# Optimization experiments

Measured on AMD Instinct MI355X. Metric: run time of the kernel, lower is better.

The kernel has to match this reference:

```python
import jax, jax.numpy as jnp
import numpy as np

DIM = 128
HEADS = 4
DIM_HEAD = 32
HIDDEN = HEADS * DIM_HEAD
SCALE = DIM_HEAD ** -0.5
EPS = 1e-5


def setup_inputs() -> dict:
    key = jax.random.key(0)
    ks = jax.random.split(key, 8)
    s = 1.0 / np.sqrt(DIM)
    x = jax.random.normal(ks[0], (32, DIM, 64, 64), dtype=jnp.float32)
    Wq = jax.random.uniform(ks[1], (HIDDEN, DIM), jnp.float32, -s, s)
    Wk = jax.random.uniform(ks[2], (HIDDEN, DIM), jnp.float32, -s, s)
    Wv = jax.random.uniform(ks[3], (HIDDEN, DIM), jnp.float32, -s, s)
    so = 1.0 / np.sqrt(HIDDEN)
    Wo = jax.random.uniform(ks[4], (DIM, HIDDEN), jnp.float32, -so, so)
    bo = jax.random.uniform(ks[5], (DIM,), jnp.float32, -so, so)
    gn_w = jnp.ones((DIM,), jnp.float32)
    gn_b = jnp.zeros((DIM,), jnp.float32)
    return {"x": x, "Wq": Wq, "Wk": Wk, "Wv": Wv, "Wo": Wo, "bo": bo,
            "gn_w": gn_w, "gn_b": gn_b}


def reference(x, Wq, Wk, Wv, Wo, bo, gn_w, gn_b):
    b, c, h, w = x.shape
    n = h * w
    xf = x.reshape(b, c, n)  # [b, c, n]
    # 1x1 convs (no bias) == channel matmuls; split heads: [b, H, d, n]
    def proj(W):
        return jnp.einsum('oc,bcn->bon', W, xf).reshape(b, HEADS, DIM_HEAD, n)
    q = proj(Wq)
    k = proj(Wk)
    v = proj(Wv)
    q = jax.nn.softmax(q, axis=-2) * SCALE  # softmax over head-dim d
    k = jax.nn.softmax(k, axis=-1)          # softmax over spatial n
    ctx = jnp.einsum('bhdn,bhen->bhde', k, v)   # [b,H,d,e], tiny d=e=32
    out = jnp.einsum('bhde,bhdn->bhen', ctx, q) # [b,H,e,n]
    out = out.reshape(b, HIDDEN, n)
    # output 1x1 conv with bias
    out = jnp.einsum('oc,bcn->bon', Wo, out) + bo[None, :, None]  # [b,dim,n]
    # GroupNorm(num_groups=1): normalize over (C, n) per sample
    mu = jnp.mean(out, axis=(1, 2), keepdims=True)
    var = jnp.var(out, axis=(1, 2), keepdims=True)
    out = (out - mu) * jax.lax.rsqrt(var + EPS)
    out = out * gn_w[None, :, None] + gn_b[None, :, None]
    return out.reshape(b, c, h, w)
```

## Files before the change

kernel.cpp:

```cpp
#include <hip/hip_runtime.h>


#define B_   32
#define C_   128
#define N_   4096
#define H_   4
#define D_   32
#define HID  128
#define NB   64
#define TPB  4
#define NSTRIP 16
#define STV  72
#define STA  136
#define SCT  40
#define SCALE 0.1767766952966369f
#define EPS  1e-5f

typedef __attribute__((ext_vector_type(8))) short short8;
typedef __attribute__((ext_vector_type(4))) short short4v;
typedef __attribute__((ext_vector_type(4))) float floatx4;

__device__ __forceinline__ short f2bf(float f) {
  unsigned u = __float_as_uint(f);
  u += 0x7FFFu + ((u >> 16) & 1u);
  return (short)(u >> 16);
}
__device__ __forceinline__ float bf2f(short h) {
  return __uint_as_float(((unsigned)(unsigned short)h) << 16);
}
__device__ __forceinline__ void gload_lds16(const float* g, void* l) {
  __builtin_amdgcn_global_load_lds(
      (const __attribute__((address_space(1))) unsigned int*)g,
      (__attribute__((address_space(3))) unsigned int*)l, 16, 0, 0);
}

__global__ __launch_bounds__(256) void k_wcast(
    const float* __restrict__ Wq, const float* __restrict__ Wk,
    const float* __restrict__ Wv, const float* __restrict__ Wo,
    short* __restrict__ wb) {
  const int i = blockIdx.x * 256 + threadIdx.x;
  const float* srcs[4] = {Wq, Wk, Wv, Wo};
#pragma unroll
  for (int m = 0; m < 4; ++m) {
    floatx4 a = ((const floatx4*)srcs[m])[i];
    short4v s = { f2bf(a[0]), f2bf(a[1]), f2bf(a[2]), f2bf(a[3]) };
    ((short4v*)(wb + m * 16384))[i] = s;
  }
}

__global__ __launch_bounds__(256, 2) void k_kv_ctx(
    const float* __restrict__ x, const short* __restrict__ Wkb,
    const short* __restrict__ Wvb, float* __restrict__ ctx_u,
    float* __restrict__ Zsum) {
  __shared__ float natx[C_ * NB];
  __shared__ short ekbuf[C_ * STV];
  __shared__ short vbuf [C_ * STV];
  const int tid = threadIdx.x;
  const int w = tid >> 6, L = tid & 63, l15 = tid & 15, q4 = (tid & 63) >> 4;
  const int b = blockIdx.x / NSTRIP;
  const int strip = blockIdx.x % NSTRIP;
  const float* xb = x + (size_t)b * C_ * N_;

  short8 ak[2][4], av[2][4];
#pragma unroll
  for (int mt = 0; mt < 2; ++mt)
#pragma unroll
    for (int ks = 0; ks < 4; ++ks) {
      ak[mt][ks] = *(const short8*)&Wkb[(w * 32 + mt * 16 + l15) * C_ + ks * 32 + q4 * 8];
      av[mt][ks] = *(const short8*)&Wvb[(w * 32 + mt * 16 + l15) * C_ + ks * 32 + q4 * 8];
    }

  const floatx4 z4 = {0.f, 0.f, 0.f, 0.f};
  floatx4 ca[2][2] = {{z4, z4}, {z4, z4}};
  float zreg[2][4] = {{0.f,0.f,0.f,0.f},{0.f,0.f,0.f,0.f}};

#pragma unroll
  for (int i = 0; i < 8; ++i) {
    const int c = w * 32 + i * 4 + (L >> 4);
    gload_lds16(xb + (size_t)c * N_ + (size_t)(strip * TPB) * NB + (L & 15) * 4,
                (char*)natx + ((w * 32 + i * 4) * NB + L * 4) * 4);
  }

  for (int t = 0; t < TPB; ++t) {
    __syncthreads();

    floatx4 acck[2][4], accv[2][4];
#pragma unroll
    for (int mt = 0; mt < 2; ++mt)
#pragma unroll
      for (int nt = 0; nt < 4; ++nt) { acck[mt][nt] = z4; accv[mt][nt] = z4; }

#pragma unroll
    for (int ks = 0; ks < 4; ++ks) {
      short8 Bf[4];
#pragma unroll
      for (int nt = 0; nt < 4; ++nt) {
        short8 s;
#pragma unroll
        for (int j = 0; j < 8; ++j)
          s[j] = f2bf(natx[(ks * 32 + q4 * 8 + j) * NB + nt * 16 + l15]);
        Bf[nt] = s;
      }
#pragma unroll
      for (int mt = 0; mt < 2; ++mt)
#pragma unroll
        for (int nt = 0; nt < 4; ++nt) {
          acck[mt][nt] = __builtin_amdgcn_mfma_f32_16x16x32_bf16(ak[mt][ks], Bf[nt], acck[mt][nt], 0, 0, 0);
          accv[mt][nt] = __builtin_amdgcn_mfma_f32_16x16x32_bf16(av[mt][ks], Bf[nt], accv[mt][nt], 0, 0, 0);
        }
    }
    __syncthreads();

    if (t + 1 < TPB) {
#pragma unroll
      for (int i = 0; i < 8; ++i) {
        const int c = w * 32 + i * 4 + (L >> 4);
        gload_lds16(xb + (size_t)c * N_ + (size_t)(strip * TPB + t + 1) * NB + (L & 15) * 4,
                    (char*)natx + ((w * 32 + i * 4) * NB + L * 4) * 4);
      }
    }

#pragma unroll
    for (int mt = 0; mt < 2; ++mt)
#pragma unroll
      for (int nt = 0; nt < 4; ++nt)
#pragma unroll
        for (int r = 0; r < 4; ++r)
          acck[mt][nt][r] = __expf(acck[mt][nt][r]);
#pragma unroll
    for (int mt = 0; mt < 2; ++mt)
#pragma unroll
      for (int r = 0; r < 4; ++r)
        zreg[mt][r] += acck[mt][0][r] + acck[mt][1][r] + acck[mt][2][r] + acck[mt][3][r];

#pragma unroll
    for (int mt = 0; mt < 2; ++mt)
#pragma unroll
      for (int nt = 0; nt < 4; ++nt)
#pragma unroll
        for (int r = 0; r < 4; ++r) {
          ekbuf[(w * 32 + mt * 16 + q4 * 4 + r) * STV + nt * 16 + l15] = f2bf(acck[mt][nt][r]);
          vbuf [(w * 32 + mt * 16 + q4 * 4 + r) * STV + nt * 16 + l15] = f2bf(accv[mt][nt][r]);
        }

#pragma unroll
    for (int ks = 0; ks < 2; ++ks) {
      short8 ae[2], be[2];
#pragma unroll
      for (int mt = 0; mt < 2; ++mt)
        ae[mt] = *(const short8*)&ekbuf[(w * 32 + mt * 16 + l15) * STV + ks * 32 + q4 * 8];
#pragma unroll
      for (int nt = 0; nt < 2; ++nt)
        be[nt] = *(const short8*)&vbuf[(w * 32 + nt * 16 + l15) * STV + ks * 32 + q4 * 8];
#pragma unroll
      for (int mt = 0; mt < 2; ++mt)
#pragma unroll
        for (int nt = 0; nt < 2; ++nt)
          ca[mt][nt] = __builtin_amdgcn_mfma_f32_16x16x32_bf16(ae[mt], be[nt], ca[mt][nt], 0, 0, 0);
    }
  }

#pragma unroll
  for (int mt = 0; mt < 2; ++mt)
#pragma unroll
    for (int r = 0; r < 4; ++r) {
      float s = zreg[mt][r];
      s += __shfl_xor(s, 1); s += __shfl_xor(s, 2);
      s += __shfl_xor(s, 4); s += __shfl_xor(s, 8);
      if (l15 == 0) atomicAdd(&Zsum[b * HID + w * 32 + mt * 16 + q4 * 4 + r], s);
    }

  float* cb = &ctx_u[((size_t)b * H_ + w) * (D_ * D_)];
#pragma unroll
  for (int mt = 0; mt < 2; ++mt)
#pragma unroll
    for (int nt = 0; nt < 2; ++nt)
#pragma unroll
      for (int r = 0; r < 4; ++r)
        atomicAdd(&cb[(mt * 16 + q4 * 4 + r) * D_ + nt * 16 + l15], ca[mt][nt][r]);
}

__global__ __launch_bounds__(256, 2) void k_q_attn_o(
    const float* __restrict__ x, const short* __restrict__ Wqb,
    const short* __restrict__ Wob, const float* __restrict__ bo,
    const float* __restrict__ ctx_u, const float* __restrict__ Zsum,
    float* __restrict__ outp, float* __restrict__ stats) {
  __shared__ float natx[C_ * NB];
  __shared__ short qat[NB * STA];
  __shared__ short ctxT[HID * SCT];
  const int tid = threadIdx.x;
  const int w = tid >> 6, L = tid & 63, l15 = tid & 15, q4 = (tid & 63) >> 4;
  const int b = blockIdx.x / NSTRIP;
  const int strip = blockIdx.x % NSTRIP;
  const float* xb = x + (size_t)b * C_ * N_;

#pragma unroll
  for (int i = 0; i < 8; ++i) {
    const int c = w * 32 + i * 4 + (L >> 4);
    gload_lds16(xb + (size_t)c * N_ + (size_t)(strip * TPB) * NB + (L & 15) * 4,
                (char*)natx + ((w * 32 + i * 4) * NB + L * 4) * 4);
  }
#pragma unroll
  for (int i = 0; i < 16; ++i) {
    const int idx = tid + i * 256;
    float v = ctx_u[(size_t)b * (H_ * D_ * D_) + idx] *
              __builtin_amdgcn_rcpf(Zsum[b * HID + (idx >> 5)]);
    ctxT[((idx >> 10) * 32 + (idx & 31)) * SCT + ((idx >> 5) & 31)] = f2bf(v);
  }

  short8 aq[2][4], ao[2][4];
#pragma unroll
  for (int mt = 0; mt < 2; ++mt)
#pragma unroll
    for (int ks = 0; ks < 4; ++ks) {
      aq[mt][ks] = *(const short8*)&Wqb[(w * 32 + mt * 16 + l15) * C_ + ks * 32 + q4 * 8];
      ao[mt][ks] = *(const short8*)&Wob[(w * 32 + mt * 16 + l15) * HID + ks * 32 + q4 * 8];
    }

  const floatx4 z4 = {0.f, 0.f, 0.f, 0.f};
  float s1 = 0.f, s2 = 0.f;

  for (int t = 0; t < TPB; ++t) {
    const int n0 = (strip * TPB + t) * NB;
    __syncthreads();

    floatx4 acc[2][4];
#pragma unroll
    for (int mt = 0; mt < 2; ++mt)
#pragma unroll
      for (int nt = 0; nt < 4; ++nt) acc[mt][nt] = z4;
#pragma unroll
    for (int ks = 0; ks < 4; ++ks) {
      short8 Bf[4];
#pragma unroll
      for (int nt = 0; nt < 4; ++nt) {
        short8 s;
#pragma unroll
        for (int j = 0; j < 8; ++j)
          s[j] = f2bf(natx[(ks * 32 + q4 * 8 + j) * NB + nt * 16 + l15]);
        Bf[nt] = s;
      }
#pragma unroll
      for (int mt = 0; mt < 2; ++mt)
#pragma unroll
        for (int nt = 0; nt < 4; ++nt)
          acc[mt][nt] = __builtin_amdgcn_mfma_f32_16x16x32_bf16(aq[mt][ks], Bf[nt], acc[mt][nt], 0, 0, 0);
    }
    __syncthreads();

    if (t + 1 < TPB) {
#pragma unroll
      for (int i = 0; i < 8; ++i) {
        const int c = w * 32 + i * 4 + (L >> 4);
        gload_lds16(xb + (size_t)c * N_ + (size_t)(n0 + NB) + (L & 15) * 4,
                    (char*)natx + ((w * 32 + i * 4) * NB + L * 4) * 4);
      }
    }

#pragma unroll
    for (int mt = 0; mt < 2; ++mt)
#pragma unroll
      for (int nt = 0; nt < 4; ++nt)
#pragma unroll
        for (int r = 0; r < 4; ++r)
          acc[mt][nt][r] = __expf(acc[mt][nt][r]);
    float inv[4];
#pragma unroll
    for (int nt = 0; nt < 4; ++nt) {
      float s = 0.f;
#pragma unroll
      for (int mt = 0; mt < 2; ++mt)
#pragma unroll
        for (int r = 0; r < 4; ++r) s += acc[mt][nt][r];
      s += __shfl_xor(s, 16); s += __shfl_xor(s, 32);
      inv[nt] = SCALE * __builtin_amdgcn_rcpf(s);
    }

#pragma unroll
    for (int mt = 0; mt < 2; ++mt)
#pragma unroll
      for (int nt = 0; nt < 4; ++nt) {
        short4v pk = { f2bf(acc[mt][nt][0] * inv[nt]), f2bf(acc[mt][nt][1] * inv[nt]),
                       f2bf(acc[mt][nt][2] * inv[nt]), f2bf(acc[mt][nt][3] * inv[nt]) };
        *(short4v*)&qat[(nt * 16 + l15) * STA + w * 32 + mt * 16 + q4 * 4] = pk;
      }

    {
      floatx4 aacc[2][4];
#pragma unroll
      for (int mt = 0; mt < 2; ++mt)
#pragma unroll
        for (int nt = 0; nt < 4; ++nt) aacc[mt][nt] = z4;
      short8 ae[2];
#pragma unroll
      for (int mt = 0; mt < 2; ++mt)
        ae[mt] = *(const short8*)&ctxT[(w * 32 + mt * 16 + l15) * SCT + q4 * 8];
#pragma unroll
      for (int nt = 0; nt < 4; ++nt) {
        short8 bq = *(const short8*)&qat[(nt * 16 + l15) * STA + w * 32 + q4 * 8];
#pragma unroll
        for (int mt = 0; mt < 2; ++mt)
          aacc[mt][nt] = __builtin_amdgcn_mfma_f32_16x16x32_bf16(ae[mt], bq, aacc[mt][nt], 0, 0, 0);
      }
#pragma unroll
      for (int nt = 0; nt < 4; ++nt)
#pragma unroll
        for (int mt = 0; mt < 2; ++mt) {
          short4v pk = { f2bf(aacc[mt][nt][0]), f2bf(aacc[mt][nt][1]),
                         f2bf(aacc[mt][nt][2]), f2bf(aacc[mt][nt][3]) };
          *(short4v*)&qat[(nt * 16 + l15) * STA + w * 32 + mt * 16 + q4 * 4] = pk;
        }
    }
    __syncthreads();

    floatx4 oacc[2][4];
#pragma unroll
    for (int mt = 0; mt < 2; ++mt)
#pragma unroll
      for (int nt = 0; nt < 4; ++nt) oacc[mt][nt] = z4;
#pragma unroll
    for (int ks = 0; ks < 4; ++ks) {
      short8 bf8[4];
#pragma unroll
      for (int nt = 0; nt < 4; ++nt)
        bf8[nt] = *(const short8*)&qat[(nt * 16 + l15) * STA + ks * 32 + q4 * 8];
#pragma unroll
      for (int mt = 0; mt < 2; ++mt)
#pragma unroll
        for (int nt = 0; nt < 4; ++nt)
          oacc[mt][nt] = __builtin_amdgcn_mfma_f32_16x16x32_bf16(ao[mt][ks], bf8[nt], oacc[mt][nt], 0, 0, 0);
    }

#pragma unroll
    for (int mt = 0; mt < 2; ++mt) {
      const int rowbase = w * 32 + mt * 16 + q4 * 4;
      const floatx4 bo4 = *(const floatx4*)&bo[rowbase];
#pragma unroll
      for (int nt = 0; nt < 4; ++nt) {
        const int n = n0 + nt * 16 + l15;
#pragma unroll
        for (int r = 0; r < 4; ++r) {
          float vv = oacc[mt][nt][r] + bo4[r];
          outp[(size_t)b * (C_ * N_) + (size_t)(rowbase + r) * N_ + n] = vv;
          s1 += vv; s2 += vv * vv;
        }
      }
    }
  }

#pragma unroll
  for (int m = 1; m < 64; m <<= 1) {
    s1 += __shfl_xor(s1, m);
    s2 += __shfl_xor(s2, m);
  }
  if ((tid & 63) == 0) {
    atomicAdd(&stats[b * 2 + 0], s1);
    atomicAdd(&stats[b * 2 + 1], s2);
  }
}

__global__ __launch_bounds__(256) void k_gnorm(
    float* __restrict__ outp, const float* __restrict__ stats,
    const float* __restrict__ gnw, const float* __restrict__ gnb) {
  const int b = blockIdx.x >> 6;
  const int blk = blockIdx.x & 63;
  const float M = (float)(C_ * N_);
  const float mu = stats[b * 2 + 0] / M;
  const float var = stats[b * 2 + 1] / M - mu * mu;
  const float rs = rsqrtf(var + EPS);
  floatx4* p = (floatx4*)(outp + (size_t)b * (C_ * N_) + (size_t)blk * 8192);
  const int tid = threadIdx.x;
#pragma unroll
  for (int i = 0; i < 8; ++i) {
    const int idx = tid + i * 256;
    const int fl = blk * 8192 + idx * 4;
    const int c = fl >> 12;
    const float wgt = gnw[c] * rs;
    const float bia = gnb[c] - mu * wgt;
    floatx4 v = p[idx];
    v[0] = v[0] * wgt + bia;
    v[1] = v[1] * wgt + bia;
    v[2] = v[2] * wgt + bia;
    v[3] = v[3] * wgt + bia;
    p[idx] = v;
  }
}

extern "C" void kernel_launch(void* const* d_in, const int* in_sizes, int n_in,
                              void* d_out, int out_size, void* d_ws, size_t ws_size,
                              hipStream_t stream) {
  (void)in_sizes; (void)n_in; (void)out_size; (void)ws_size;
  const float* x   = (const float*)d_in[0];
  const float* Wq  = (const float*)d_in[1];
  const float* Wk  = (const float*)d_in[2];
  const float* Wv  = (const float*)d_in[3];
  const float* Wo  = (const float*)d_in[4];
  const float* bo  = (const float*)d_in[5];
  const float* gnw = (const float*)d_in[6];
  const float* gnb = (const float*)d_in[7];
  float* outp  = (float*)d_out;
  float* ctx_u = (float*)d_ws;
  float* Zsum  = ctx_u + B_ * H_ * D_ * D_;
  float* stats = Zsum + B_ * HID;
  short* wb    = (short*)(stats + B_ * 2);
  const size_t zbytes = (size_t)(B_ * H_ * D_ * D_ + B_ * HID + B_ * 2) * sizeof(float);
  hipMemsetAsync(d_ws, 0, zbytes, stream);
  hipLaunchKernelGGL(k_wcast,    dim3(64),           dim3(256), 0, stream, Wq, Wk, Wv, Wo, wb);
  hipLaunchKernelGGL(k_kv_ctx,   dim3(B_ * NSTRIP),  dim3(256), 0, stream, x, wb + 16384, wb + 32768, ctx_u, Zsum);
  hipLaunchKernelGGL(k_q_attn_o, dim3(B_ * NSTRIP),  dim3(256), 0, stream, x, wb, wb + 49152, bo, ctx_u, Zsum, outp, stats);
  hipLaunchKernelGGL(k_gnorm,    dim3(B_ * 64),      dim3(256), 0, stream, outp, stats, gnw, gnb);
}
```

Baseline: 205.0 us.

## Stash swizzled bf16 transposed x in first pass for reuse by Q kernel

The KV/context kernel now writes its bf16-converted, transposed x tiles to a workspace buffer, and the Q/attention/output kernel reads that half-size buffer instead of re-reading and re-converting fp32 x. Both LDS layouts get an XOR swizzle to reduce bank conflicts. The second kernel uses smaller strips (more blocks) and a higher occupancy bound. This adds extra global writes in the first kernel and depends on the workspace being large enough, falling back to the legacy path otherwise.

```diff
diff --git a/kernel.cpp b/kernel.cpp
--- a/kernel.cpp
+++ b/kernel.cpp
@@ -10,6 +10,8 @@
 #define NB   64
 #define TPB  4
 #define NSTRIP 16
+#define TPB2   2
+#define NSTRIP2 32
 #define STV  72
 #define STA  136
 #define SCT  40
@@ -32,6 +34,9 @@
   __builtin_amdgcn_global_load_lds(
       (const __attribute__((address_space(1))) unsigned int*)g,
       (__attribute__((address_space(3))) unsigned int*)l, 16, 0, 0);
+}
+__device__ __forceinline__ int swzn(int c) {
+  return (((c >> 3) & 1) << 4) | (((c >> 4) & 1) << 3);
 }
 
 __global__ __launch_bounds__(256) void k_wcast(
@@ -51,7 +56,7 @@
 __global__ __launch_bounds__(256, 2) void k_kv_ctx(
     const float* __restrict__ x, const short* __restrict__ Wkb,
     const short* __restrict__ Wvb, float* __restrict__ ctx_u,
-    float* __restrict__ Zsum) {
+    float* __restrict__ Zsum, short* __restrict__ xt) {
   __shared__ float natx[C_ * NB];
   __shared__ short ekbuf[C_ * STV];
   __shared__ short vbuf [C_ * STV];
@@ -60,6 +65,8 @@
   const int b = blockIdx.x / NSTRIP;
   const int strip = blockIdx.x % NSTRIP;
   const float* xb = x + (size_t)b * C_ * N_;
+  const int szr = ((q4 & 1) << 4) | ((q4 & 2) << 2);
+  const int szw = (l15 & 7) << 3;
 
   short8 ak[2][4], av[2][4];
 #pragma unroll
@@ -77,7 +84,7 @@
 #pragma unroll
   for (int i = 0; i < 8; ++i) {
     const int c = w * 32 + i * 4 + (L >> 4);
-    gload_lds16(xb + (size_t)c * N_ + (size_t)(strip * TPB) * NB + (L & 15) * 4,
+    gload_lds16(xb + (size_t)c * N_ + (size_t)(strip * TPB) * NB + (((L & 15) * 4) ^ swzn(c)),
                 (char*)natx + ((w * 32 + i * 4) * NB + L * 4) * 4);
   }
 
@@ -90,6 +97,7 @@
 #pragma unroll
       for (int nt = 0; nt < 4; ++nt) { acck[mt][nt] = z4; accv[mt][nt] = z4; }
 
+    short8 myB[4];
 #pragma unroll
     for (int ks = 0; ks < 4; ++ks) {
       short8 Bf[4];
@@ -98,8 +106,11 @@
         short8 s;
 #pragma unroll
         for (int j = 0; j < 8; ++j)
-          s[j] = f2bf(natx[(ks * 32 + q4 * 8 + j) * NB + nt * 16 + l15]);
+          s[j] = f2bf(natx[(ks * 32 + q4 * 8 + j) * NB + ((nt * 16 + l15) ^ szr)]);
         Bf[nt] = s;
+      }
+      if (ks == w) {
+        myB[0] = Bf[0]; myB[1] = Bf[1]; myB[2] = Bf[2]; myB[3] = Bf[3];
       }
 #pragma unroll
       for (int mt = 0; mt < 2; ++mt)
@@ -115,9 +126,16 @@
 #pragma unroll
       for (int i = 0; i < 8; ++i) {
         const int c = w * 32 + i * 4 + (L >> 4);
-        gload_lds16(xb + (size_t)c * N_ + (size_t)(strip * TPB + t + 1) * NB + (L & 15) * 4,
+        gload_lds16(xb + (size_t)c * N_ + (size_t)(strip * TPB + t + 1) * NB + (((L & 15) * 4) ^ swzn(c)),
                     (char*)natx + ((w * 32 + i * 4) * NB + L * 4) * 4);
       }
+    }
+
+    if (xt) {
+      short* xtb = xt + ((size_t)(b * 64 + strip * TPB + t)) * 8192;
+#pragma unroll
+      for (int nt = 0; nt < 4; ++nt)
+        *(short8*)&xtb[(nt * 16 + l15) * C_ + ((w * 32 + q4 * 8) ^ szw)] = myB[nt];
     }
 
 #pragma unroll
@@ -180,7 +198,180 @@
         atomicAdd(&cb[(mt * 16 + q4 * 4 + r) * D_ + nt * 16 + l15], ca[mt][nt][r]);
 }
 
-__global__ __launch_bounds__(256, 2) void k_q_attn_o(
+__global__ __launch_bounds__(256, 3) void k_q_attn_o(
+    const short* __restrict__ xt, const short* __restrict__ Wqb,
+    const short* __restrict__ Wob, const float* __restrict__ bo,
+    const float* __restrict__ ctx_u, const float* __restrict__ Zsum,
+    float* __restrict__ outp, float* __restrict__ stats) {
+  __shared__ short natx2[NB * C_];
+  __shared__ short qat[NB * STA];
+  __shared__ short ctxT[HID * SCT];
+  const int tid = threadIdx.x;
+  const int w = tid >> 6, L = tid & 63, l15 = tid & 15, q4 = (tid & 63) >> 4;
+  const int b = blockIdx.x / NSTRIP2;
+  const int strip = blockIdx.x % NSTRIP2;
+  const int szw = (l15 & 7) << 3;
+  (void)L;
+
+  {
+    const float* src = (const float*)(xt + (size_t)(b * 64 + strip * TPB2) * 8192);
+#pragma unroll
+    for (int i = 0; i < 4; ++i)
+      gload_lds16(src + tid * 4 + i * 1024, (char*)natx2 + tid * 16 + i * 4096);
+  }
+#pragma unroll
+  for (int i = 0; i < 16; ++i) {
+    const int idx = tid + i * 256;
+    float v = ctx_u[(size_t)b * (H_ * D_ * D_) + idx] *
+              __builtin_amdgcn_rcpf(Zsum[b * HID + (idx >> 5)]);
+    ctxT[((idx >> 10) * 32 + (idx & 31)) * SCT + ((idx >> 5) & 31)] = f2bf(v);
+  }
+
+  short8 aq[2][4], ao[2][4];
+#pragma unroll
+  for (int mt = 0; mt < 2; ++mt)
+#pragma unroll
+    for (int ks = 0; ks < 4; ++ks) {
+      aq[mt][ks] = *(const short8*)&Wqb[(w * 32 + mt * 16 + l15) * C_ + ks * 32 + q4 * 8];
+      ao[mt][ks] = *(const short8*)&Wob[(w * 32 + mt * 16 + l15) * HID + ks * 32 + q4 * 8];
+    }
+
+  const floatx4 z4 = {0.f, 0.f, 0.f, 0.f};
+  float s1 = 0.f, s2 = 0.f;
+
+  for (int t = 0; t < TPB2; ++t) {
+    const int n0 = (strip * TPB2 + t) * NB;
+    __syncthreads();
+
+    floatx4 acc[2][4];
+#pragma unroll
+    for (int mt = 0; mt < 2; ++mt)
+#pragma unroll
+      for (int nt = 0; nt < 4; ++nt) acc[mt][nt] = z4;
+#pragma unroll
+    for (int ks = 0; ks < 4; ++ks) {
+      short8 Bf[4];
+#pragma unroll
+      for (int nt = 0; nt < 4; ++nt)
+        Bf[nt] = *(const short8*)&natx2[(nt * 16 + l15) * C_ + ((ks * 32 + q4 * 8) ^ szw)];
+#pragma unroll
+      for (int mt = 0; mt < 2; ++mt)
+#pragma unroll
+        for (int nt = 0; nt < 4; ++nt)
+          acc[mt][nt] = __builtin_amdgcn_mfma_f32_16x16x32_bf16(aq[mt][ks], Bf[nt], acc[mt][nt], 0, 0, 0);
+    }
+    __syncthreads();
+
+    if (t + 1 < TPB2) {
+      const float* src = (const float*)(xt + (size_t)(b * 64 + strip * TPB2 + t + 1) * 8192);
+#pragma unroll
+      for (int i = 0; i < 4; ++i)
+        gload_lds16(src + tid * 4 + i * 1024, (char*)natx2 + tid * 16 + i * 4096);
+    }
+
+#pragma unroll
+    for (int mt = 0; mt < 2; ++mt)
+#pragma unroll
+      for (int nt = 0; nt < 4; ++nt)
+#pragma unroll
+        for (int r = 0; r < 4; ++r)
+          acc[mt][nt][r] = __expf(acc[mt][nt][r]);
+    float inv[4];
+#pragma unroll
+    for (int nt = 0; nt < 4; ++nt) {
+      float s = 0.f;
+#pragma unroll
+      for (int mt = 0; mt < 2; ++mt)
+#pragma unroll
+        for (int r = 0; r < 4; ++r) s += acc[mt][nt][r];
+      s += __shfl_xor(s, 16); s += __shfl_xor(s, 32);
+      inv[nt] = SCALE * __builtin_amdgcn_rcpf(s);
+    }
+
+#pragma unroll
+    for (int mt = 0; mt < 2; ++mt)
+#pragma unroll
+      for (int nt = 0; nt < 4; ++nt) {
+        short4v pk = { f2bf(acc[mt][nt][0] * inv[nt]), f2bf(acc[mt][nt][1] * inv[nt]),
+                       f2bf(acc[mt][nt][2] * inv[nt]), f2bf(acc[mt][nt][3] * inv[nt]) };
+        *(short4v*)&qat[(nt * 16 + l15) * STA + w * 32 + mt * 16 + q4 * 4] = pk;
+      }
+
+    {
+      floatx4 aacc[2][4];
+#pragma unroll
+      for (int mt = 0; mt < 2; ++mt)
+#pragma unroll
+        for (int nt = 0; nt < 4; ++nt) aacc[mt][nt] = z4;
+      short8 ae[2];
+#pragma unroll
+      for (int mt = 0; mt < 2; ++mt)
+        ae[mt] = *(const short8*)&ctxT[(w * 32 + mt * 16 + l15) * SCT + q4 * 8];
+#pragma unroll
+      for (int nt = 0; nt < 4; ++nt) {
+        short8 bq = *(const short8*)&qat[(nt * 16 + l15) * STA + w * 32 + q4 * 8];
+#pragma unroll
+        for (int mt = 0; mt < 2; ++mt)
+          aacc[mt][nt] = __builtin_amdgcn_mfma_f32_16x16x32_bf16(ae[mt], bq, aacc[mt][nt], 0, 0, 0);
+      }
+#pragma unroll
+      for (int nt = 0; nt < 4; ++nt)
+#pragma unroll
+        for (int mt = 0; mt < 2; ++mt) {
+          short4v pk = { f2bf(aacc[mt][nt][0]), f2bf(aacc[mt][nt][1]),
+                         f2bf(aacc[mt][nt][2]), f2bf(aacc[mt][nt][3]) };
+          *(short4v*)&qat[(nt * 16 + l15) * STA + w * 32 + mt * 16 + q4 * 4] = pk;
+        }
+    }
+    __syncthreads();
+
+    floatx4 oacc[2][4];
+#pragma unroll
+    for (int mt = 0; mt < 2; ++mt)
+#pragma unroll
+      for (int nt = 0; nt < 4; ++nt) oacc[mt][nt] = z4;
+#pragma unroll
+    for (int ks = 0; ks < 4; ++ks) {
+      short8 bf8[4];
+#pragma unroll
+      for (int nt = 0; nt < 4; ++nt)
+        bf8[nt] = *(const short8*)&qat[(nt * 16 + l15) * STA + ks * 32 + q4 * 8];
+#pragma unroll
+      for (int mt = 0; mt < 2; ++mt)
+#pragma unroll
+        for (int nt = 0; nt < 4; ++nt)
+          oacc[mt][nt] = __builtin_amdgcn_mfma_f32_16x16x32_bf16(ao[mt][ks], bf8[nt], oacc[mt][nt], 0, 0, 0);
+    }
+
+#pragma unroll
+    for (int mt = 0; mt < 2; ++mt) {
+      const int rowbase = w * 32 + mt * 16 + q4 * 4;
+      const floatx4 bo4 = *(const floatx4*)&bo[rowbase];
+#pragma unroll
+      for (int nt = 0; nt < 4; ++nt) {
+        const int n = n0 + nt * 16 + l15;
+#pragma unroll
+        for (int r = 0; r < 4; ++r) {
+          float vv = oacc[mt][nt][r] + bo4[r];
+          outp[(size_t)b * (C_ * N_) + (size_t)(rowbase + r) * N_ + n] = vv;
+          s1 += vv; s2 += vv * vv;
+        }
+      }
+    }
+  }
+
+#pragma unroll
+  for (int m = 1; m < 64; m <<= 1) {
+    s1 += __shfl_xor(s1, m);
+    s2 += __shfl_xor(s2, m);
+  }
+  if ((tid & 63) == 0) {
+    atomicAdd(&stats[b * 2 + 0], s1);
+    atomicAdd(&stats[b * 2 + 1], s2);
+  }
+}
+
+__global__ __launch_bounds__(256, 2) void k_q_attn_o_legacy(
     const float* __restrict__ x, const short* __restrict__ Wqb,
     const short* __restrict__ Wob, const float* __restrict__ bo,
     const float* __restrict__ ctx_u, const float* __restrict__ Zsum,
@@ -389,7 +580,7 @@
 extern "C" void kernel_launch(void* const* d_in, const int* in_sizes, int n_in,
                               void* d_out, int out_size, void* d_ws, size_t ws_size,
                               hipStream_t stream) {
-  (void)in_sizes; (void)n_in; (void)out_size; (void)ws_size;
+  (void)in_sizes; (void)n_in; (void)out_size;
   const float* x   = (const float*)d_in[0];
   const float* Wq  = (const float*)d_in[1];
   const float* Wk  = (const float*)d_in[2];
@@ -403,10 +594,18 @@
   float* Zsum  = ctx_u + B_ * H_ * D_ * D_;
   float* stats = Zsum + B_ * HID;
   short* wb    = (short*)(stats + B_ * 2);
+  short* xt    = (short*)((char*)d_ws + 672000);
+  const int fast = ws_size >= (size_t)34226432;
   const size_t zbytes = (size_t)(B_ * H_ * D_ * D_ + B_ * HID + B_ * 2) * sizeof(float);
   hipMemsetAsync(d_ws, 0, zbytes, stream);
-  hipLaunchKernelGGL(k_wcast,    dim3(64),           dim3(256), 0, stream, Wq, Wk, Wv, Wo, wb);
-  hipLaunchKernelGGL(k_kv_ctx,   dim3(B_ * NSTRIP),  dim3(256), 0, stream, x, wb + 16384, wb + 32768, ctx_u, Zsum);
-  hipLaunchKernelGGL(k_q_attn_o, dim3(B_ * NSTRIP),  dim3(256), 0, stream, x, wb, wb + 49152, bo, ctx_u, Zsum, outp, stats);
-  hipLaunchKernelGGL(k_gnorm,    dim3(B_ * 64),      dim3(256), 0, stream, outp, stats, gnw, gnb);
-}
+  hipLaunchKernelGGL(k_wcast,  dim3(64),          dim3(256), 0, stream, Wq, Wk, Wv, Wo, wb);
+  hipLaunchKernelGGL(k_kv_ctx, dim3(B_ * NSTRIP), dim3(256), 0, stream, x, wb + 16384, wb + 32768,
+                     ctx_u, Zsum, fast ? xt : (short*)nullptr);
+  if (fast)
+    hipLaunchKernelGGL(k_q_attn_o, dim3(B_ * NSTRIP2), dim3(256), 0, stream,
+                       xt, wb, wb + 49152, bo, ctx_u, Zsum, outp, stats);
+  else
+    hipLaunchKernelGGL(k_q_attn_o_legacy, dim3(B_ * NSTRIP), dim3(256), 0, stream,
+                       x, wb, wb + 49152, bo, ctx_u, Zsum, outp, stats);
+  hipLaunchKernelGGL(k_gnorm, dim3(B_ * 64), dim3(256), 0, stream, outp, stats, gnw, gnb);
+}
```

New measurement: 315.5 us. 53.9% more time.

## Pre-cast x to bf16 MFMA-fragment layout once, reuse in both attention kernels

Applied to the files above, without the earlier changes.

Adds a kernel that converts x to bf16 once and writes it in a tile layout that matches the MFMA B-fragment order. Both the KV-context and Q/attention/output kernels then load half-size tiles straight into LDS and read fragments with a single vector load, with no per-element float-to-bf16 conversion. With the smaller LDS tile, the kernels raise their occupancy hint to 3 blocks per SM. The Q kernel is split into twice as many strips of half the length. The cost is an extra launch plus a full write and re-read of a bf16 copy of x through global memory.

```diff
diff --git a/kernel.cpp b/kernel.cpp
--- a/kernel.cpp
+++ b/kernel.cpp
@@ -10,6 +10,8 @@
 #define NB   64
 #define TPB  4
 #define NSTRIP 16
+#define TPB2   2
+#define NSTRIP2 32
 #define STV  72
 #define STA  136
 #define SCT  40
@@ -24,9 +26,6 @@
   unsigned u = __float_as_uint(f);
   u += 0x7FFFu + ((u >> 16) & 1u);
   return (short)(u >> 16);
-}
-__device__ __forceinline__ float bf2f(short h) {
-  return __uint_as_float(((unsigned)(unsigned short)h) << 16);
 }
 __device__ __forceinline__ void gload_lds16(const float* g, void* l) {
   __builtin_amdgcn_global_load_lds(
@@ -48,18 +47,36 @@
   }
 }
 
-__global__ __launch_bounds__(256, 2) void k_kv_ctx(
-    const float* __restrict__ x, const short* __restrict__ Wkb,
+__global__ __launch_bounds__(256) void k_xcast(
+    const float* __restrict__ x, short* __restrict__ xt) {
+  const int tile = blockIdx.x;
+  const int b = tile >> 6, tn = tile & 63;
+  const int tid = threadIdx.x;
+  const int ks = tid >> 6, L = tid & 63, l15 = L & 15, q4 = L >> 4;
+  const float* xb = x + (size_t)b * (C_ * N_) + (size_t)(ks * 32 + q4 * 8) * N_
+                      + tn * NB + l15;
+  short* xtb = xt + (size_t)tile * 8192 + (size_t)(ks * 256 + L) * 8;
+#pragma unroll
+  for (int nt = 0; nt < 4; ++nt) {
+    short8 s;
+#pragma unroll
+    for (int j = 0; j < 8; ++j)
+      s[j] = f2bf(xb[(size_t)j * N_ + nt * 16]);
+    *(short8*)&xtb[nt * 512] = s;
+  }
+}
+
+__global__ __launch_bounds__(256, 3) void k_kv_ctx(
+    const short* __restrict__ xt, const short* __restrict__ Wkb,
     const short* __restrict__ Wvb, float* __restrict__ ctx_u,
     float* __restrict__ Zsum) {
-  __shared__ float natx[C_ * NB];
+  __shared__ short natx2[8192];
   __shared__ short ekbuf[C_ * STV];
   __shared__ short vbuf [C_ * STV];
   const int tid = threadIdx.x;
   const int w = tid >> 6, L = tid & 63, l15 = tid & 15, q4 = (tid & 63) >> 4;
   const int b = blockIdx.x / NSTRIP;
   const int strip = blockIdx.x % NSTRIP;
-  const float* xb = x + (size_t)b * C_ * N_;
 
   short8 ak[2][4], av[2][4];
 #pragma unroll
@@ -74,11 +91,11 @@
   floatx4 ca[2][2] = {{z4, z4}, {z4, z4}};
   float zreg[2][4] = {{0.f,0.f,0.f,0.f},{0.f,0.f,0.f,0.f}};
 
-#pragma unroll
-  for (int i = 0; i < 8; ++i) {
-    const int c = w * 32 + i * 4 + (L >> 4);
-    gload_lds16(xb + (size_t)c * N_ + (size_t)(strip * TPB) * NB + (L & 15) * 4,
-                (char*)natx + ((w * 32 + i * 4) * NB + L * 4) * 4);
+  {
+    const float* src = (const float*)(xt + (size_t)(b * 64 + strip * TPB) * 8192);
+#pragma unroll
+    for (int i = 0; i < 4; ++i)
+      gload_lds16(src + tid * 4 + i * 1024, (char*)natx2 + tid * 16 + i * 4096);
   }
 
   for (int t = 0; t < TPB; ++t) {
@@ -94,13 +111,8 @@
     for (int ks = 0; ks < 4; ++ks) {
       short8 Bf[4];
 #pragma unroll
-      for (int nt = 0; nt < 4; ++nt) {
-        short8 s;
-#pragma unroll
-        for (int j = 0; j < 8; ++j)
-          s[j] = f2bf(natx[(ks * 32 + q4 * 8 + j) * NB + nt * 16 + l15]);
-        Bf[nt] = s;
-      }
+      for (int nt = 0; nt < 4; ++nt)
+        Bf[nt] = *(const short8*)&natx2[((ks * 4 + nt) * 64 + L) * 8];
 #pragma unroll
       for (int mt = 0; mt < 2; ++mt)
 #pragma unroll
@@ -112,12 +124,10 @@
     __syncthreads();
 
     if (t + 1 < TPB) {
-#pragma unroll
-      for (int i = 0; i < 8; ++i) {
-        const int c = w * 32 + i * 4 + (L >> 4);
-        gload_lds16(xb + (size_t)c * N_ + (size_t)(strip * TPB + t + 1) * NB + (L & 15) * 4,
-                    (char*)natx + ((w * 32 + i * 4) * NB + L * 4) * 4);
-      }
+      const float* src = (const float*)(xt + (size_t)(b * 64 + strip * TPB + t + 1) * 8192);
+#pragma unroll
+      for (int i = 0; i < 4; ++i)
+        gload_lds16(src + tid * 4 + i * 1024, (char*)natx2 + tid * 16 + i * 4096);
     }
 
 #pragma unroll
@@ -180,25 +190,24 @@
         atomicAdd(&cb[(mt * 16 + q4 * 4 + r) * D_ + nt * 16 + l15], ca[mt][nt][r]);
 }
 
-__global__ __launch_bounds__(256, 2) void k_q_attn_o(
-    const float* __restrict__ x, const short* __restrict__ Wqb,
+__global__ __launch_bounds__(256, 3) void k_q_attn_o(
+    const short* __restrict__ xt, const short* __restrict__ Wqb,
     const short* __restrict__ Wob, const float* __restrict__ bo,
     const float* __restrict__ ctx_u, const float* __restrict__ Zsum,
     float* __restrict__ outp, float* __restrict__ stats) {
-  __shared__ float natx[C_ * NB];
+  __shared__ short natx2[8192];
   __shared__ short qat[NB * STA];
   __shared__ short ctxT[HID * SCT];
   const int tid = threadIdx.x;
   const int w = tid >> 6, L = tid & 63, l15 = tid & 15, q4 = (tid & 63) >> 4;
-  const int b = blockIdx.x / NSTRIP;
-  const int strip = blockIdx.x % NSTRIP;
-  const float* xb = x + (size_t)b * C_ * N_;
-
-#pragma unroll
-  for (int i = 0; i < 8; ++i) {
-    const int c = w * 32 + i * 4 + (L >> 4);
-    gload_lds16(xb + (size_t)c * N_ + (size_t)(strip * TPB) * NB + (L & 15) * 4,
-                (char*)natx + ((w * 32 + i * 4) * NB + L * 4) * 4);
+  const int b = blockIdx.x / NSTRIP2;
+  const int strip = blockIdx.x % NSTRIP2;
+
+  {
+    const float* src = (const float*)(xt + (size_t)(b * 64 + strip * TPB2) * 8192);
+#pragma unroll
+    for (int i = 0; i < 4; ++i)
+      gload_lds16(src + tid * 4 + i * 1024, (char*)natx2 + tid * 16 + i * 4096);
   }
 #pragma unroll
   for (int i = 0; i < 16; ++i) {
@@ -220,8 +229,8 @@
   const floatx4 z4 = {0.f, 0.f, 0.f, 0.f};
   float s1 = 0.f, s2 = 0.f;
 
-  for (int t = 0; t < TPB; ++t) {
-    const int n0 = (strip * TPB + t) * NB;
+  for (int t = 0; t < TPB2; ++t) {
+    const int n0 = (strip * TPB2 + t) * NB;
     __syncthreads();
 
     floatx4 acc[2][4];
@@ -233,13 +242,8 @@
     for (int ks = 0; ks < 4; ++ks) {
       short8 Bf[4];
 #pragma unroll
-      for (int nt = 0; nt < 4; ++nt) {
-        short8 s;
-#pragma unroll
-        for (int j = 0; j < 8; ++j)
-          s[j] = f2bf(natx[(ks * 32 + q4 * 8 + j) * NB + nt * 16 + l15]);
-        Bf[nt] = s;
-      }
+      for (int nt = 0; nt < 4; ++nt)
+        Bf[nt] = *(const short8*)&natx2[((ks * 4 + nt) * 64 + L) * 8];
 #pragma unroll
       for (int mt = 0; mt < 2; ++mt)
 #pragma unroll
@@ -248,13 +252,11 @@
     }
     __syncthreads();
 
-    if (t + 1 < TPB) {
-#pragma unroll
-      for (int i = 0; i < 8; ++i) {
-        const int c = w * 32 + i * 4 + (L >> 4);
-        gload_lds16(xb + (size_t)c * N_ + (size_t)(n0 + NB) + (L & 15) * 4,
-                    (char*)natx + ((w * 32 + i * 4) * NB + L * 4) * 4);
-      }
+    if (t + 1 < TPB2) {
+      const float* src = (const float*)(xt + (size_t)(b * 64 + strip * TPB2 + t + 1) * 8192);
+#pragma unroll
+      for (int i = 0; i < 4; ++i)
+        gload_lds16(src + tid * 4 + i * 1024, (char*)natx2 + tid * 16 + i * 4096);
     }
 
 #pragma unroll
@@ -403,10 +405,12 @@
   float* Zsum  = ctx_u + B_ * H_ * D_ * D_;
   float* stats = Zsum + B_ * HID;
   short* wb    = (short*)(stats + B_ * 2);
+  short* xt    = (short*)((char*)d_ws + 672000);
   const size_t zbytes = (size_t)(B_ * H_ * D_ * D_ + B_ * HID + B_ * 2) * sizeof(float);
   hipMemsetAsync(d_ws, 0, zbytes, stream);
   hipLaunchKernelGGL(k_wcast,    dim3(64),           dim3(256), 0, stream, Wq, Wk, Wv, Wo, wb);
-  hipLaunchKernelGGL(k_kv_ctx,   dim3(B_ * NSTRIP),  dim3(256), 0, stream, x, wb + 16384, wb + 32768, ctx_u, Zsum);
-  hipLaunchKernelGGL(k_q_attn_o, dim3(B_ * NSTRIP),  dim3(256), 0, stream, x, wb, wb + 49152, bo, ctx_u, Zsum, outp, stats);
+  hipLaunchKernelGGL(k_xcast,    dim3(B_ * 64),      dim3(256), 0, stream, x, xt);
+  hipLaunchKernelGGL(k_kv_ctx,   dim3(B_ * NSTRIP),  dim3(256), 0, stream, xt, wb + 16384, wb + 32768, ctx_u, Zsum);
+  hipLaunchKernelGGL(k_q_attn_o, dim3(B_ * NSTRIP2), dim3(256), 0, stream, xt, wb, wb + 49152, bo, ctx_u, Zsum, outp, stats);
   hipLaunchKernelGGL(k_gnorm,    dim3(B_ * 64),      dim3(256), 0, stream, outp, stats, gnw, gnb);
 }
```

Result: slower. 268.2 us (+30.8%).

## Load x into registers, convert to bf16 MFMA fragments once in LDS

Applied to the files above, without the earlier changes.

Replaces the direct global-to-LDS fp32 staging of x with per-thread register loads. Each thread converts its values to bf16 and writes them in MFMA B-fragment order, so the inner loop does one vector LDS read per fragment. The old path did eight strided LDS reads plus conversions per fragment. The next tile is register-prefetched one iteration ahead, and LDS for x is halved, allowing launch bounds of 3 blocks per SM. The cost is more register pressure from the 32-float prefetch buffer, which could spill under the tighter occupancy bound.

```diff
diff --git a/kernel.cpp b/kernel.cpp
--- a/kernel.cpp
+++ b/kernel.cpp
@@ -25,14 +25,22 @@
   u += 0x7FFFu + ((u >> 16) & 1u);
   return (short)(u >> 16);
 }
-__device__ __forceinline__ float bf2f(short h) {
-  return __uint_as_float(((unsigned)(unsigned short)h) << 16);
-}
-__device__ __forceinline__ void gload_lds16(const float* g, void* l) {
-  __builtin_amdgcn_global_load_lds(
-      (const __attribute__((address_space(1))) unsigned int*)g,
-      (__attribute__((address_space(3))) unsigned int*)l, 16, 0, 0);
-}
+
+#define XLOAD(tt)                                                        \
+  _Pragma("unroll")                                                      \
+  for (int nt = 0; nt < 4; ++nt)                                         \
+    _Pragma("unroll")                                                    \
+    for (int j = 0; j < 8; ++j)                                          \
+      xr[nt][j] = xw[(size_t)j * N_ + (size_t)(tt) * NB + nt * 16];
+
+#define XCVT(fragbuf)                                                    \
+  _Pragma("unroll")                                                      \
+  for (int nt = 0; nt < 4; ++nt) {                                       \
+    short8 s;                                                            \
+    _Pragma("unroll")                                                    \
+    for (int j = 0; j < 8; ++j) s[j] = f2bf(xr[nt][j]);                  \
+    *(short8*)&fragbuf[((w * 4 + nt) * 64 + L) * 8] = s;                 \
+  }
 
 __global__ __launch_bounds__(256) void k_wcast(
     const float* __restrict__ Wq, const float* __restrict__ Wk,
@@ -48,18 +56,19 @@
   }
 }
 
-__global__ __launch_bounds__(256, 2) void k_kv_ctx(
+__global__ __launch_bounds__(256, 3) void k_kv_ctx(
     const float* __restrict__ x, const short* __restrict__ Wkb,
     const short* __restrict__ Wvb, float* __restrict__ ctx_u,
     float* __restrict__ Zsum) {
-  __shared__ float natx[C_ * NB];
+  __shared__ short frag[8192];
   __shared__ short ekbuf[C_ * STV];
   __shared__ short vbuf [C_ * STV];
   const int tid = threadIdx.x;
   const int w = tid >> 6, L = tid & 63, l15 = tid & 15, q4 = (tid & 63) >> 4;
   const int b = blockIdx.x / NSTRIP;
   const int strip = blockIdx.x % NSTRIP;
-  const float* xb = x + (size_t)b * C_ * N_;
+  const float* xw = x + (size_t)b * (C_ * N_) + (size_t)(w * 32 + q4 * 8) * N_
+                      + (size_t)(strip * TPB) * NB + l15;
 
   short8 ak[2][4], av[2][4];
 #pragma unroll
@@ -73,13 +82,11 @@
   const floatx4 z4 = {0.f, 0.f, 0.f, 0.f};
   floatx4 ca[2][2] = {{z4, z4}, {z4, z4}};
   float zreg[2][4] = {{0.f,0.f,0.f,0.f},{0.f,0.f,0.f,0.f}};
-
-#pragma unroll
-  for (int i = 0; i < 8; ++i) {
-    const int c = w * 32 + i * 4 + (L >> 4);
-    gload_lds16(xb + (size_t)c * N_ + (size_t)(strip * TPB) * NB + (L & 15) * 4,
-                (char*)natx + ((w * 32 + i * 4) * NB + L * 4) * 4);
-  }
+  float xr[4][8];
+
+  XLOAD(0)
+  XCVT(frag)
+  XLOAD(1)
 
   for (int t = 0; t < TPB; ++t) {
     __syncthreads();
@@ -94,13 +101,8 @@
     for (int ks = 0; ks < 4; ++ks) {
       short8 Bf[4];
 #pragma unroll
-      for (int nt = 0; nt < 4; ++nt) {
-        short8 s;
-#pragma unroll
-        for (int j = 0; j < 8; ++j)
-          s[j] = f2bf(natx[(ks * 32 + q4 * 8 + j) * NB + nt * 16 + l15]);
-        Bf[nt] = s;
-      }
+      for (int nt = 0; nt < 4; ++nt)
+        Bf[nt] = *(const short8*)&frag[((ks * 4 + nt) * 64 + L) * 8];
 #pragma unroll
       for (int mt = 0; mt < 2; ++mt)
 #pragma unroll
@@ -112,12 +114,8 @@
     __syncthreads();
 
     if (t + 1 < TPB) {
-#pragma unroll
-      for (int i = 0; i < 8; ++i) {
-        const int c = w * 32 + i * 4 + (L >> 4);
-        gload_lds16(xb + (size_t)c * N_ + (size_t)(strip * TPB + t + 1) * NB + (L & 15) * 4,
-                    (char*)natx + ((w * 32 + i * 4) * NB + L * 4) * 4);
-      }
+      XCVT(frag)
+      if (t + 2 < TPB) { XLOAD(t + 2) }
     }
 
 #pragma unroll
@@ -180,26 +178,25 @@
         atomicAdd(&cb[(mt * 16 + q4 * 4 + r) * D_ + nt * 16 + l15], ca[mt][nt][r]);
 }
 
-__global__ __launch_bounds__(256, 2) void k_q_attn_o(
+__global__ __launch_bounds__(256, 3) void k_q_attn_o(
     const float* __restrict__ x, const short* __restrict__ Wqb,
     const short* __restrict__ Wob, const float* __restrict__ bo,
     const float* __restrict__ ctx_u, const float* __restrict__ Zsum,
     float* __restrict__ outp, float* __restrict__ stats) {
-  __shared__ float natx[C_ * NB];
+  __shared__ short frag[8192];
   __shared__ short qat[NB * STA];
   __shared__ short ctxT[HID * SCT];
   const int tid = threadIdx.x;
   const int w = tid >> 6, L = tid & 63, l15 = tid & 15, q4 = (tid & 63) >> 4;
   const int b = blockIdx.x / NSTRIP;
   const int strip = blockIdx.x % NSTRIP;
-  const float* xb = x + (size_t)b * C_ * N_;
-
-#pragma unroll
-  for (int i = 0; i < 8; ++i) {
-    const int c = w * 32 + i * 4 + (L >> 4);
-    gload_lds16(xb + (size_t)c * N_ + (size_t)(strip * TPB) * NB + (L & 15) * 4,
-                (char*)natx + ((w * 32 + i * 4) * NB + L * 4) * 4);
-  }
+  const float* xw = x + (size_t)b * (C_ * N_) + (size_t)(w * 32 + q4 * 8) * N_
+                      + (size_t)(strip * TPB) * NB + l15;
+
+  float xr[4][8];
+  XLOAD(0)
+  XCVT(frag)
+  XLOAD(1)
 #pragma unroll
   for (int i = 0; i < 16; ++i) {
     const int idx = tid + i * 256;
@@ -233,13 +230,8 @@
     for (int ks = 0; ks < 4; ++ks) {
       short8 Bf[4];
 #pragma unroll
-      for (int nt = 0; nt < 4; ++nt) {
-        short8 s;
-#pragma unroll
-        for (int j = 0; j < 8; ++j)
-          s[j] = f2bf(natx[(ks * 32 + q4 * 8 + j) * NB + nt * 16 + l15]);
-        Bf[nt] = s;
-      }
+      for (int nt = 0; nt < 4; ++nt)
+        Bf[nt] = *(const short8*)&frag[((ks * 4 + nt) * 64 + L) * 8];
 #pragma unroll
       for (int mt = 0; mt < 2; ++mt)
 #pragma unroll
@@ -249,12 +241,8 @@
     __syncthreads();
 
     if (t + 1 < TPB) {
-#pragma unroll
-      for (int i = 0; i < 8; ++i) {
-        const int c = w * 32 + i * 4 + (L >> 4);
-        gload_lds16(xb + (size_t)c * N_ + (size_t)(n0 + NB) + (L & 15) * 4,
-                    (char*)natx + ((w * 32 + i * 4) * NB + L * 4) * 4);
-      }
+      XCVT(frag)
+      if (t + 2 < TPB) { XLOAD(t + 2) }
     }
 
 #pragma unroll
@@ -405,8 +393,8 @@
   short* wb    = (short*)(stats + B_ * 2);
   const size_t zbytes = (size_t)(B_ * H_ * D_ * D_ + B_ * HID + B_ * 2) * sizeof(float);
   hipMemsetAsync(d_ws, 0, zbytes, stream);
-  hipLaunchKernelGGL(k_wcast,    dim3(64),           dim3(256), 0, stream, Wq, Wk, Wv, Wo, wb);
-  hipLaunchKernelGGL(k_kv_ctx,   dim3(B_ * NSTRIP),  dim3(256), 0, stream, x, wb + 16384, wb + 32768, ctx_u, Zsum);
-  hipLaunchKernelGGL(k_q_attn_o, dim3(B_ * NSTRIP),  dim3(256), 0, stream, x, wb, wb + 49152, bo, ctx_u, Zsum, outp, stats);
-  hipLaunchKernelGGL(k_gnorm,    dim3(B_ * 64),      dim3(256), 0, stream, outp, stats, gnw, gnb);
-}
+  hipLaunchKernelGGL(k_wcast,    dim3(64),          dim3(256), 0, stream, Wq, Wk, Wv, Wo, wb);
+  hipLaunchKernelGGL(k_kv_ctx,   dim3(B_ * NSTRIP), dim3(256), 0, stream, x, wb + 16384, wb + 32768, ctx_u, Zsum);
+  hipLaunchKernelGGL(k_q_attn_o, dim3(B_ * NSTRIP), dim3(256), 0, stream, x, wb, wb + 49152, bo, ctx_u, Zsum, outp, stats);
+  hipLaunchKernelGGL(k_gnorm,    dim3(B_ * 64),     dim3(256), 0, stream, outp, stats, gnw, gnb);
+}
```

Result: slower. 278.6 us (+35.9%).
